# Kernel optimization log

Hardware: AMD Instinct MI355X
Metric: run time of the kernel (lower is better)

Reference implementation:

```python
import jax, jax.numpy as jnp
import numpy as np

NC = 80          # num_classes
REG_MAX = 16
TOPK = 10
IMG = 640
STRIDES = (8, 16, 32)
EPS = 1e-9


def make_anchors(shapes, strides):
    pts, strs = [], []
    for (h, w), s in zip(shapes, strides):
        sx = jnp.arange(w, dtype=jnp.float32)  # grid_cell_offset = 0.0
        sy = jnp.arange(h, dtype=jnp.float32)
        gy, gx = jnp.meshgrid(sy, sx, indexing='ij')
        pts.append(jnp.stack([gx, gy], -1).reshape(-1, 2))
        strs.append(jnp.full((h * w, 1), float(s), dtype=jnp.float32))
    return jnp.concatenate(pts, 0), jnp.concatenate(strs, 0)  # [A,2], [A,1]


def ciou(box1, box2, eps=1e-7):
    # boxes are xyxy, broadcastable; returns CIoU with last dim squeezed
    b1x1, b1y1, b1x2, b1y2 = jnp.split(box1, 4, -1)
    b2x1, b2y1, b2x2, b2y2 = jnp.split(box2, 4, -1)
    w1, h1 = b1x2 - b1x1, b1y2 - b1y1
    w2, h2 = b2x2 - b2x1, b2y2 - b2y1
    inter = (jnp.clip(jnp.minimum(b1x2, b2x2) - jnp.maximum(b1x1, b2x1), 0.0)
             * jnp.clip(jnp.minimum(b1y2, b2y2) - jnp.maximum(b1y1, b2y1), 0.0))
    union = w1 * h1 + w2 * h2 - inter + eps
    iou = inter / union
    cw = jnp.maximum(b1x2, b2x2) - jnp.minimum(b1x1, b2x1)
    ch = jnp.maximum(b1y2, b2y2) - jnp.minimum(b1y1, b2y1)
    c2 = cw ** 2 + ch ** 2 + eps
    rho2 = ((b2x1 + b2x2 - b1x1 - b1x2) ** 2 + (b2y1 + b2y2 - b1y1 - b1y2) ** 2) / 4.0
    v = (4.0 / np.pi ** 2) * (jnp.arctan(w2 / (h2 + eps)) - jnp.arctan(w1 / (h1 + eps))) ** 2
    alpha = jax.lax.stop_gradient(v / (v - iou + (1.0 + eps)))
    return (iou - (rho2 / c2 + v * alpha))[..., 0]


def bbox_decode(anchor_points, pred_distri):
    # distribution-focal decode: softmax over REG_MAX bins, expectation, dist2bbox
    B, A, _ = pred_distri.shape
    pd = pred_distri.reshape(B, A, 4, REG_MAX)
    proj = jnp.arange(REG_MAX, dtype=jnp.float32)
    dist = jnp.einsum('bacr,r->bac', jax.nn.softmax(pd, -1), proj)  # [B,A,4] ltrb
    lt, rb = dist[..., :2], dist[..., 2:]
    return jnp.concatenate([anchor_points - lt, anchor_points + rb], -1)  # xyxy


def assigner(pd_scores, pd_bboxes, anc_points, gt_labels, gt_bboxes, mask_gt,
             alpha=0.5, beta=6.0):
    # pd_scores [B,A,C] (sigmoid), pd_bboxes [B,A,4], gt_* [B,M,...], mask_gt [B,M,1]
    B, A, C = pd_scores.shape
    M = gt_bboxes.shape[1]
    mask_gt = mask_gt.astype(jnp.float32)
    # anchors whose center lies inside each gt box
    lt = anc_points[None, None, :, :] - gt_bboxes[:, :, None, :2]   # [B,M,A,2]
    rb = gt_bboxes[:, :, None, 2:] - anc_points[None, None, :, :]
    mask_in_gts = (jnp.minimum(lt.min(-1), rb.min(-1)) > EPS).astype(jnp.float32)  # [B,M,A]
    mask = mask_in_gts * mask_gt
    # class score of each anchor at the gt's label
    sc = jnp.take_along_axis(pd_scores[:, None, :, :],
                             gt_labels[:, :, None, None].astype(jnp.int32), axis=-1)[..., 0]  # [B,M,A]
    overlaps = jnp.clip(ciou(gt_bboxes[:, :, None, :], pd_bboxes[:, None, :, :]), 0.0) * mask
    bbox_scores = sc * mask
    align_metric = (bbox_scores ** alpha) * (overlaps ** beta)  # [B,M,A]
    # top-k candidates per gt
    _, idxs = jax.lax.top_k(align_metric, TOPK)                 # [B,M,K]
    valid = jnp.broadcast_to(mask_gt > 0, (B, M, TOPK))
    idxs = jnp.where(valid, idxs, 0)
    cnt = jnp.zeros((B * M, A), jnp.float32).at[
        jnp.arange(B * M)[:, None], idxs.reshape(B * M, TOPK)
    ].add(valid.reshape(B * M, TOPK).astype(jnp.float32)).reshape(B, M, A)
    mask_topk = jnp.where(cnt > 1, 0.0, cnt)
    mask_pos = mask_topk * mask_in_gts * mask_gt               # [B,M,A]
    # resolve anchors assigned to multiple gts by max overlap
    fg = mask_pos.sum(1)                                       # [B,A]
    multi = fg[:, None, :] > 1
    is_max = jax.nn.one_hot(overlaps.argmax(1), M, dtype=jnp.float32).transpose(0, 2, 1)
    mask_pos = jnp.where(multi, is_max, mask_pos)
    fg_mask = mask_pos.sum(1)                                  # [B,A]
    tgt_idx = mask_pos.argmax(1)                               # [B,A]
    # gather targets
    flat = tgt_idx + jnp.arange(B)[:, None] * M
    t_labels = jnp.clip(gt_labels.reshape(-1)[flat], 0)        # [B,A]
    t_bboxes = gt_bboxes.reshape(-1, 4)[flat]                  # [B,A,4]
    t_scores = jax.nn.one_hot(t_labels, C, dtype=jnp.float32) * (fg_mask[..., None] > 0)
    # normalize scores by aligned metric
    am = align_metric * mask_pos
    pos_am = am.max(-1, keepdims=True)                         # [B,M,1]
    pos_ov = (overlaps * mask_pos).max(-1, keepdims=True)      # [B,M,1]
    norm = (am * pos_ov / (pos_am + EPS)).max(1)[..., None]    # [B,A,1]
    return t_bboxes, t_scores * norm, fg_mask > 0


def setup_inputs() -> dict:
    key = jax.random.key(0)
    ks = jax.random.split(key, 9)
    B, M = 16, 32
    inp = {
        'cls0': jax.random.normal(ks[0], (B, NC, 80, 80), jnp.float32),
        'cls1': jax.random.normal(ks[1], (B, NC, 40, 40), jnp.float32),
        'cls2': jax.random.normal(ks[2], (B, NC, 20, 20), jnp.float32),
        'reg0': jax.random.normal(ks[3], (B, 4 * REG_MAX, 80, 80), jnp.float32),
        'reg1': jax.random.normal(ks[4], (B, 4 * REG_MAX, 40, 40), jnp.float32),
        'reg2': jax.random.normal(ks[5], (B, 4 * REG_MAX, 20, 20), jnp.float32),
    }
    cxy = jax.random.uniform(ks[6], (B, M, 2), minval=0.1, maxval=0.9)
    wh = jax.random.uniform(ks[7], (B, M, 2), minval=0.02, maxval=0.25)
    inp['boxes'] = jnp.concatenate([cxy, wh], -1)  # normalized cxcywh
    inp['labels'] = jax.random.randint(ks[8], (B, M), 0, NC)
    return inp


def reference(cls0, cls1, cls2, reg0, reg1, reg2, boxes, labels):
    cls_out, reg_out = [cls0, cls1, cls2], [reg0, reg1, reg2]
    B = cls0.shape[0]
    anc, stride_t = make_anchors([r.shape[2:] for r in reg_out], STRIDES)
    pred_scores = jnp.concatenate(
        [c.transpose(0, 2, 3, 1).reshape(B, -1, NC) for c in cls_out], 1)        # [B,A,C]
    pred_distri = jnp.concatenate(
        [r.transpose(0, 2, 3, 1).reshape(B, -1, 4 * REG_MAX) for r in reg_out], 1)
    # gt2xyxy: normalized cxcywh -> pixel xyxy
    cx, cy, w, h = jnp.split(boxes, 4, -1)
    gt_bboxes = jnp.concatenate([(cx - w / 2) * IMG, (cy - h / 2) * IMG,
                                 (cx + w / 2) * IMG, (cy + h / 2) * IMG], -1)
    mask_gt = gt_bboxes.sum(2, keepdims=True) > 0.0
    pred_bboxes = bbox_decode(anc, pred_distri)                                   # anchor units
    sg = jax.lax.stop_gradient
    t_bboxes, t_scores, fg_mask = assigner(
        sg(jax.nn.sigmoid(pred_scores)), sg(pred_bboxes) * stride_t,
        anc * stride_t, labels, gt_bboxes, mask_gt)
    tss = jnp.maximum(t_scores.sum(), 1.0)
    # classification BCE-with-logits
    x, t = pred_scores, t_scores
    bce = jnp.maximum(x, 0.0) - x * t + jnp.log1p(jnp.exp(-jnp.abs(x)))
    l_cls = bce.sum() / tss
    # bbox CIoU loss
    t_bboxes = t_bboxes / stride_t
    weight = t_scores.sum(-1) * fg_mask                                           # [B,A]
    iou = ciou(pred_bboxes, t_bboxes)
    l_iou = ((1.0 - iou) * weight).sum() / tss
    # DFL loss
    tltrb = jnp.clip(jnp.concatenate([anc - t_bboxes[..., :2],
                                      t_bboxes[..., 2:] - anc], -1),
                     0.0, REG_MAX - 1 - 0.01)                                     # [B,A,4]
    logp = jax.nn.log_softmax(pred_distri.reshape(B, -1, 4, REG_MAX), -1)
    tl = jnp.floor(tltrb).astype(jnp.int32)
    wl = (tl + 1).astype(jnp.float32) - tltrb
    lp_tl = jnp.take_along_axis(logp, tl[..., None], -1)[..., 0]
    lp_tr = jnp.take_along_axis(logp, (tl + 1)[..., None], -1)[..., 0]
    dfl = (-(lp_tl * wl + lp_tr * (1.0 - wl))).mean(-1)                           # [B,A]
    l_dfl = (dfl * weight).sum() / tss
    loss = jnp.stack([0.5 * l_cls, 7.5 * l_iou, 1.5 * l_dfl])
    return loss.sum(), loss
```

## Files before the change

kernel.cpp:

```cpp
#include <hip/hip_runtime.h>

#define NB 16
#define NM 32
#define NA 8400
#define NCC 80
#define NREG 64
#define A0 6400
#define A1 1600
#define A2 400
#define CAP 768

#define PRE_GRID 1024
#define PL_GRID 525

#define ACC_STRIDE 16
#define ACC_SLOTS 4


__device__ __forceinline__ void anch(int a, float& ax, float& ay, float& s, int& lvl, int& p) {
  if (a < A0)            { lvl = 0; p = a;          s = 8.f;  ax = (float)(p % 80); ay = (float)(p / 80); }
  else if (a < A0 + A1)  { lvl = 1; p = a - A0;     s = 16.f; ax = (float)(p % 40); ay = (float)(p / 40); }
  else                   { lvl = 2; p = a - A0 - A1; s = 32.f; ax = (float)(p % 20); ay = (float)(p / 20); }
}

__device__ __forceinline__ float cls_at(const float* c0, const float* c1, const float* c2,
                                        int b, int ch, int a) {
  if (a < A0)           return c0[((size_t)(b * NCC + ch)) * A0 + a];
  if (a < A0 + A1)      return c1[((size_t)(b * NCC + ch)) * A1 + (a - A0)];
  return c2[((size_t)(b * NCC + ch)) * A2 + (a - A0 - A1)];
}

__device__ __forceinline__ float reg_at(const float* r0, const float* r1, const float* r2,
                                        int b, int ch, int lvl, int p) {
  if (lvl == 0) return r0[((size_t)(b * NREG + ch)) * A0 + p];
  if (lvl == 1) return r1[((size_t)(b * NREG + ch)) * A1 + p];
  return r2[((size_t)(b * NREG + ch)) * A2 + p];
}

__device__ __forceinline__ void gtbox(const float* boxes, int b, int m,
                                      float& x1, float& y1, float& x2, float& y2, bool& valid) {
  const float* q = boxes + ((size_t)(b * NM + m)) * 4;
  float cx = q[0], cy = q[1], w = q[2], h = q[3];
  x1 = (cx - w * 0.5f) * 640.f; y1 = (cy - h * 0.5f) * 640.f;
  x2 = (cx + w * 0.5f) * 640.f; y2 = (cy + h * 0.5f) * 640.f;
  valid = (x1 + y1 + x2 + y2) > 0.f;
}

__device__ __forceinline__ float ciou_f(float b1x1, float b1y1, float b1x2, float b1y2,
                                        float b2x1, float b2y1, float b2x2, float b2y2) {
  const float eps = 1e-7f;
  float w1 = b1x2 - b1x1, h1 = b1y2 - b1y1;
  float w2 = b2x2 - b2x1, h2 = b2y2 - b2y1;
  float iw = fmaxf(fminf(b1x2, b2x2) - fmaxf(b1x1, b2x1), 0.f);
  float ih = fmaxf(fminf(b1y2, b2y2) - fmaxf(b1y1, b2y1), 0.f);
  float inter = iw * ih;
  float uni = w1 * h1 + w2 * h2 - inter + eps;
  float iou = inter / uni;
  float cw = fmaxf(b1x2, b2x2) - fminf(b1x1, b2x1);
  float ch = fmaxf(b1y2, b2y2) - fminf(b1y1, b2y1);
  float c2 = cw * cw + ch * ch + eps;
  float dx = b2x1 + b2x2 - b1x1 - b1x2;
  float dy = b2y1 + b2y2 - b1y1 - b1y2;
  float rho2 = (dx * dx + dy * dy) * 0.25f;
  float at = atanf(w2 / (h2 + eps)) - atanf(w1 / (h1 + eps));
  float v = 0.4052847345693511f * at * at;
  float alpha = v / (v - iou + (1.0f + eps));
  return iou - (rho2 / c2 + v * alpha);
}

__device__ __forceinline__ float align_of(float sc, float o) {
  float o2 = o * o, o4 = o2 * o2;
  return sqrtf(sc) * (o2 * o4);
}

__device__ __forceinline__ float softplus_fast(float x) {
  float e = __expf(-fabsf(x));
  return fmaxf(x, 0.f) + __logf(1.f + e);
}


__global__ __launch_bounds__(256) void k_pre(
    const float* r0, const float* r1, const float* r2,
    const float* c0, const float* c1, const float* c2,
    float4* bb, float4* mls, int* fgcnt, int* msum,
    unsigned* pos_am, unsigned* pos_ov, double* acc, double* bce_part) {
  const int gtid = blockIdx.x * 256 + threadIdx.x;
  const int nthr = gridDim.x * 256;

  for (int t = gtid; t < NB * NA; t += nthr) {
    fgcnt[t] = 0; msum[t] = 0;
    if (t < NB * NM) { pos_am[t] = 0u; pos_ov[t] = 0u; }
    if (t < ACC_SLOTS * ACC_STRIDE) acc[t] = 0.0;

    int b = t / NA, a = t % NA;
    float ax, ay, s; int lvl, p;
    anch(a, ax, ay, s, lvl, p);
    const float* rg; int HW;
    if (lvl == 0) { rg = r0; HW = A0; }
    else if (lvl == 1) { rg = r1; HW = A1; }
    else { rg = r2; HW = A2; }
    const float* base = rg + ((size_t)b * NREG) * HW + p;
    float dist[4], ml[4];
    for (int sd = 0; sd < 4; ++sd) {
      float x[16]; float mx = -1e30f;
      for (int r = 0; r < 16; ++r) { x[r] = base[(size_t)(sd * 16 + r) * HW]; mx = fmaxf(mx, x[r]); }
      float se = 0.f, wsum = 0.f;
      for (int r = 0; r < 16; ++r) { float e = __expf(x[r] - mx); se += e; wsum += e * (float)r; }
      dist[sd] = wsum / se;
      ml[sd] = mx + __logf(se);
    }
    bb[t]  = make_float4(ax - dist[0], ay - dist[1], ax + dist[2], ay + dist[3]);
    mls[t] = make_float4(ml[0], ml[1], ml[2], ml[3]);
  }

  const size_t N0 = (size_t)NB * NCC * A0 / 4;
  const size_t N1 = (size_t)NB * NCC * A1 / 4;
  const size_t N2 = (size_t)NB * NCC * A2 / 4;
  const size_t NT = N0 + N1 + N2;
  const float4* f0 = (const float4*)c0;
  const float4* f1 = (const float4*)c1;
  const float4* f2 = (const float4*)c2;
  float s0 = 0.f, s1 = 0.f;
  for (size_t i = (size_t)gtid; i < NT; i += (size_t)nthr) {
    float4 v;
    if (i < N0) v = f0[i];
    else if (i < N0 + N1) v = f1[i - N0];
    else v = f2[i - N0 - N1];
    s0 += softplus_fast(v.x) + softplus_fast(v.z);
    s1 += softplus_fast(v.y) + softplus_fast(v.w);
  }
  __shared__ double sred[256];
  sred[threadIdx.x] = (double)(s0 + s1);
  __syncthreads();
  for (int off = 128; off; off >>= 1) {
    if (threadIdx.x < off) sred[threadIdx.x] += sred[threadIdx.x + off];
    __syncthreads();
  }
  if (threadIdx.x == 0) bce_part[blockIdx.x] = sred[0];
}


__global__ __launch_bounds__(256) void k_assign(
    const float* boxes, const int* labels, const float4* bb,
    const float* c0, const float* c1, const float* c2,
    int* fgcnt, int* msum) {
  __shared__ float sv[CAP];
  __shared__ int   si[CAP];
  __shared__ int   s_n;
  const int bm = blockIdx.x;
  const int b = bm / NM, m = bm % NM;
  const int tid = threadIdx.x;
  const int lane = tid & 63;

  float gx1, gy1, gx2, gy2; bool valid;
  gtbox(boxes, b, m, gx1, gy1, gx2, gy2, valid);
  if (!valid) return;
  int lbl = labels[bm]; if (lbl < 0) lbl = 0; if (lbl >= NCC) lbl = NCC - 1;
  if (tid == 0) s_n = 0;
  __syncthreads();

  const int   Ws[3]   = {80, 40, 20};
  const float ss[3]   = {8.f, 16.f, 32.f};
  const int   loff[3] = {0, A0, A0 + A1};
  int rx0[3], ry0[3], rw[3], bc[3];
  int total = 0;
  for (int l = 0; l < 3; ++l) {
    float s = ss[l]; int W = Ws[l];
    int ax0 = (int)floorf((gx1 + 1e-9f) / s);
    int ax1 = (int)ceilf((gx2 - 1e-9f) / s);
    int ay0 = (int)floorf((gy1 + 1e-9f) / s);
    int ay1 = (int)ceilf((gy2 - 1e-9f) / s);
    ax0 = max(ax0, 0); ay0 = max(ay0, 0);
    ax1 = min(ax1, W - 1); ay1 = min(ay1, W - 1);
    rx0[l] = ax0; ry0[l] = ay0;
    rw[l] = max(0, ax1 - ax0 + 1);
    int rhl = max(0, ay1 - ay0 + 1);
    bc[l] = total;
    total += rw[l] * rhl;
  }
  int iters = (total + 255) >> 8;
  for (int it = 0; it < iters; ++it) {
    int idx = it * 256 + tid;
    bool pred = false; float am = 0.f; int a = 0;
    if (idx < total) {
      int l = (idx >= bc[2]) ? 2 : ((idx >= bc[1]) ? 1 : 0);
      int r = idx - bc[l];
      int iy = r / rw[l], ix = r - iy * rw[l];
      int axg = rx0[l] + ix, ayg = ry0[l] + iy;
      a = loff[l] + ayg * Ws[l] + axg;
      float s = ss[l];
      float axp = (float)axg * s, ayp = (float)ayg * s;
      float mn = fminf(fminf(axp - gx1, ayp - gy1), fminf(gx2 - axp, gy2 - ayp));
      if (mn > 1e-9f) {
        pred = true;
        float4 pb = bb[(size_t)b * NA + a];
        float c = ciou_f(gx1, gy1, gx2, gy2, pb.x * s, pb.y * s, pb.z * s, pb.w * s);
        float o = fmaxf(c, 0.f);
        float x = cls_at(c0, c1, c2, b, lbl, a);
        float sc = 1.f / (1.f + expf(-x));
        am = align_of(sc, o);
      }
    }
    unsigned long long mask = __ballot(pred);
    if (mask) {
      int nact = __popcll(mask);
      int leader = __ffsll(mask) - 1;
      int basec = 0;
      if (lane == leader) basec = atomicAdd(&s_n, nact);
      basec = __shfl(basec, leader);
      if (pred) {
        int off = basec + __popcll(mask & ((1ull << lane) - 1ull));
        if (off < CAP) { sv[off] = am; si[off] = a; }
      }
    }
  }
  __syncthreads();
  int n = s_n; if (n > CAP) n = CAP;
  if (n == 0) return;
  if (tid >= 64) return;

  float v[12]; int ix[12];
#pragma unroll
  for (int k = 0; k < 12; ++k) {
    int j = k * 64 + tid;
    bool in = (j < n);
    v[k]  = in ? sv[j] : -2.f;
    ix[k] = in ? si[j] : (1 << 30);
  }
  int cnt = 0;
#pragma unroll
  for (int k = 0; k < 12; ++k) cnt += (v[k] > 0.f) ? 1 : 0;
  for (int o = 32; o; o >>= 1) cnt += __shfl_xor(cnt, o);
  int npos = cnt;

  if (npos > 10) {
    for (int p = 0; p < 10; ++p) {
      float bv = -1.f; int bi = 1 << 30;
#pragma unroll
      for (int k = 0; k < 12; ++k) {
        if (v[k] > bv || (v[k] == bv && ix[k] < bi)) { bv = v[k]; bi = ix[k]; }
      }
      for (int o = 32; o; o >>= 1) {
        float wv = __shfl_xor(bv, o); int wi = __shfl_xor(bi, o);
        if (wv > bv || (wv == bv && wi < bi)) { bv = wv; bi = wi; }
      }
#pragma unroll
      for (int k = 0; k < 12; ++k) if (ix[k] == bi) v[k] = -1.f;
      if (tid == 0) {
        atomicAdd(&fgcnt[(size_t)b * NA + bi], 1);
        atomicAdd(&msum[(size_t)b * NA + bi], m);
      }
    }
  } else {
#pragma unroll
    for (int k = 0; k < 12; ++k) {
      if (v[k] > 0.f) {
        atomicAdd(&fgcnt[(size_t)b * NA + ix[k]], 1);
        atomicAdd(&msum[(size_t)b * NA + ix[k]], m);
      }
    }
    int need = 10 - npos;
    for (int j = tid; j < n; j += 64) {
      if (sv[j] == 0.f) {
        int i = si[j];
        if (i < 10) {
          int pb = 0;
          for (int q = 0; q < n; ++q) pb += (sv[q] > 0.f && si[q] < i) ? 1 : 0;
          if (i - pb < need) {
            atomicAdd(&fgcnt[(size_t)b * NA + i], 1);
            atomicAdd(&msum[(size_t)b * NA + i], m);
          }
        }
      }
    }
  }
}


__global__ __launch_bounds__(256) void k_resolve(const float* boxes, const int* labels,
                                                 const float4* bb,
                                                 const float* c0, const float* c1, const float* c2,
                                                 const int* fgcnt, const int* msum,
                                                 int* assign, float* amv,
                                                 unsigned* pos_am, unsigned* pos_ov) {
  int t = blockIdx.x * blockDim.x + threadIdx.x;
  if (t >= NB * NA) return;
  int b = t / NA, a = t % NA;
  int fg = fgcnt[t];
  int asn = -1; float o = 0.f;
  if (fg > 0) {
    float ax, ay, s; int lvl, p;
    anch(a, ax, ay, s, lvl, p);
    float axp = ax * s, ayp = ay * s;
    float4 pb = bb[t];
    float px1 = pb.x * s, py1 = pb.y * s, px2 = pb.z * s, py2 = pb.w * s;
    if (fg == 1) {
      asn = msum[t];
      float gx1, gy1, gx2, gy2; bool valid;
      gtbox(boxes, b, asn, gx1, gy1, gx2, gy2, valid);
      o = fmaxf(ciou_f(gx1, gy1, gx2, gy2, px1, py1, px2, py2), 0.f);
    } else {
      float bv = -1e30f; int bi = 0;
      for (int m = 0; m < NM; ++m) {
        float gx1, gy1, gx2, gy2; bool valid;
        gtbox(boxes, b, m, gx1, gy1, gx2, gy2, valid);
        float om = 0.f;
        if (valid) {
          float mn = fminf(fminf(axp - gx1, ayp - gy1), fminf(gx2 - axp, gy2 - ayp));
          if (mn > 1e-9f)
            om = fmaxf(ciou_f(gx1, gy1, gx2, gy2, px1, py1, px2, py2), 0.f);
        }
        if (om > bv) { bv = om; bi = m; }
      }
      asn = bi; o = bv;
    }
    float am = 0.f;
    if (o > 0.f) {
      int lbl = labels[b * NM + asn]; if (lbl < 0) lbl = 0; if (lbl >= NCC) lbl = NCC - 1;
      float x = cls_at(c0, c1, c2, b, lbl, a);
      float sc = 1.f / (1.f + expf(-x));
      am = align_of(sc, o);
      atomicMax(&pos_am[b * NM + asn], __float_as_uint(am));
      atomicMax(&pos_ov[b * NM + asn], __float_as_uint(o));
    }
    amv[t] = am;
  }
  assign[t] = asn;
}


__global__ __launch_bounds__(256) void k_post(const float* c0, const float* c1, const float* c2,
    const float* r0, const float* r1, const float* r2,
    const float* boxes, const int* labels, const int* assign, const float* amv,
    const float4* bb, const float4* mls, const unsigned* pos_am, const unsigned* pos_ov,
    double* acc) {
  const int tid = threadIdx.x;
  const int t = blockIdx.x * 256 + tid;
  double t_norm = 0.0, t_x = 0.0, t_iou = 0.0, t_dfl = 0.0;
  int asn = (t < NB * NA) ? assign[t] : -1;
  if (asn >= 0) {
    int b = t / NA, a = t % NA;
    float pam = __uint_as_float(pos_am[b * NM + asn]);
    float pov = __uint_as_float(pos_ov[b * NM + asn]);
    float norm = amv[t] * pov / (pam + 1e-9f);
    int lbl = labels[b * NM + asn]; if (lbl < 0) lbl = 0; if (lbl >= NCC) lbl = NCC - 1;
    float x = cls_at(c0, c1, c2, b, lbl, a);
    float gx1, gy1, gx2, gy2; bool valid;
    gtbox(boxes, b, asn, gx1, gy1, gx2, gy2, valid);
    float ax, ay, s; int lvl, p;
    anch(a, ax, ay, s, lvl, p);
    float inv_s = 1.f / s;
    float tx1 = gx1 * inv_s, ty1 = gy1 * inv_s, tx2 = gx2 * inv_s, ty2 = gy2 * inv_s;
    float4 pb = bb[t];
    float iou = ciou_f(pb.x, pb.y, pb.z, pb.w, tx1, ty1, tx2, ty2);
    float4 ml = mls[t];
    float tgt[4] = { ax - tx1, ay - ty1, tx2 - ax, ty2 - ay };
    float mlv[4] = { ml.x, ml.y, ml.z, ml.w };
    float dfl = 0.f;
    for (int sd = 0; sd < 4; ++sd) {
      float tv = fminf(fmaxf(tgt[sd], 0.f), 14.99f);
      float tlf = floorf(tv);
      int tl = (int)tlf;
      float wl = (tlf + 1.f) - tv;
      float xtl = reg_at(r0, r1, r2, b, sd * 16 + tl,     lvl, p);
      float xtr = reg_at(r0, r1, r2, b, sd * 16 + tl + 1, lvl, p);
      dfl += -((xtl - mlv[sd]) * wl + (xtr - mlv[sd]) * (1.f - wl));
    }
    dfl *= 0.25f;
    t_norm = (double)norm;
    t_x    = (double)(norm * x);
    t_iou  = (double)((1.f - iou) * norm);
    t_dfl  = (double)(dfl * norm);
  }
  __shared__ double sred[256];
  double vals[4] = { t_norm, t_x, t_iou, t_dfl };
  for (int q = 0; q < 4; ++q) {
    sred[tid] = vals[q];
    __syncthreads();
    for (int off = 128; off; off >>= 1) {
      if (tid < off) sred[tid] += sred[tid + off];
      __syncthreads();
    }
    if (tid == 0 && sred[0] != 0.0) atomicAdd(&acc[q * ACC_STRIDE], sred[0]);
    __syncthreads();
  }
}


__global__ __launch_bounds__(256) void k_final(const double* bce_part, const double* acc, float* out) {
  __shared__ double sred[256];
  double s = 0.0;
  for (int i = threadIdx.x; i < PRE_GRID; i += 256) s += bce_part[i];
  sred[threadIdx.x] = s;
  __syncthreads();
  for (int off = 128; off; off >>= 1) {
    if (threadIdx.x < off) sred[threadIdx.x] += sred[threadIdx.x + off];
    __syncthreads();
  }
  if (threadIdx.x == 0) {
    double a_bce  = sred[0];
    double a_norm = acc[0 * ACC_STRIDE];
    double a_x    = acc[1 * ACC_STRIDE];
    double a_iou  = acc[2 * ACC_STRIDE];
    double a_dfl  = acc[3 * ACC_STRIDE];
    double tss = a_norm; if (tss < 1.0) tss = 1.0;
    double l0 = 0.5 * (a_bce - a_x) / tss;
    double l1 = 7.5 * a_iou / tss;
    double l2 = 1.5 * a_dfl / tss;
    out[0] = (float)(l0 + l1 + l2);
    out[1] = (float)l0;
    out[2] = (float)l1;
    out[3] = (float)l2;
  }
}


extern "C" void kernel_launch(void* const* d_in, const int* in_sizes, int n_in,
                              void* d_out, int out_size, void* d_ws, size_t ws_size,
                              hipStream_t stream) {
  (void)in_sizes; (void)n_in; (void)out_size; (void)ws_size;
  const float* cls0  = (const float*)d_in[0];
  const float* cls1  = (const float*)d_in[1];
  const float* cls2  = (const float*)d_in[2];
  const float* reg0  = (const float*)d_in[3];
  const float* reg1  = (const float*)d_in[4];
  const float* reg2  = (const float*)d_in[5];
  const float* boxes = (const float*)d_in[6];
  const int*   labels = (const int*)d_in[7];
  float* out = (float*)d_out;

  const size_t BA = (size_t)NB * NA;
  const int    BM = NB * NM;

  char* wsb = (char*)d_ws;
  double*   bce_part = (double*)wsb;
  double*   acc      = bce_part + PRE_GRID;
  unsigned* pos_am   = (unsigned*)(acc + ACC_SLOTS * ACC_STRIDE);
  unsigned* pos_ov   = pos_am + BM;
  int*      fgcnt    = (int*)(pos_ov + BM);
  int*      msum     = fgcnt + BA;
  float*    bbp      = (float*)(msum + BA);
  float*    mlsp     = bbp + BA * 4;
  float*    amv      = mlsp + BA * 4;
  int*      assign   = (int*)(amv + BA);

  float4* bb  = (float4*)bbp;
  float4* mls = (float4*)mlsp;

  k_pre<<<PRE_GRID, 256, 0, stream>>>(reg0, reg1, reg2, cls0, cls1, cls2,
                                      bb, mls, fgcnt, msum, pos_am, pos_ov,
                                      acc, bce_part);
  k_assign<<<BM, 256, 0, stream>>>(boxes, labels, (const float4*)bb,
                                   cls0, cls1, cls2, fgcnt, msum);
  k_resolve<<<PL_GRID, 256, 0, stream>>>(boxes, labels, (const float4*)bb, cls0, cls1, cls2,
                                         fgcnt, msum, assign, amv, pos_am, pos_ov);
  k_post<<<PL_GRID, 256, 0, stream>>>(cls0, cls1, cls2, reg0, reg1, reg2,
                                      boxes, labels, assign, amv,
                                      (const float4*)bb, (const float4*)mls, pos_am, pos_ov,
                                      acc);
  k_final<<<1, 256, 0, stream>>>(bce_part, acc, out);
}
```

Before: 67.69 us.

## Compact foreground anchors into a worklist and fuse resolve/post via per-GT accumulators

The assign kernel now pushes each newly-touched foreground anchor onto a global worklist. A single small-grid kernel then resolves and scores only those anchors instead of scanning all B*A anchors twice. The per-anchor normalization by pos_am/pos_ov is deferred by accumulating am-weighted sums per GT and scaling them in the final kernel, which removes the need for a separate post pass. The pre kernel also processes four anchors per thread using float4 loads of the regression logits. Risks: worklist overflow is silently capped at WL_MAX, there is extra atomic traffic on double accumulators, and the per-GT deferred scaling is only equivalent to the original norm if pos_am/pos_ov are final before scaling (they are, since scaling happens in k_final).

```diff
diff --git a/kernel.cpp b/kernel.cpp
--- a/kernel.cpp
+++ b/kernel.cpp
@@ -11,10 +11,8 @@
 #define CAP 768
 
 #define PRE_GRID 1024
-#define PL_GRID 525
-
-#define ACC_STRIDE 16
-#define ACC_SLOTS 4
+#define WL_MAX 5376
+#define RP_GRID 20
 
 
 __device__ __forceinline__ void anch(int a, float& ax, float& ay, float& s, int& lvl, int& p) {
@@ -83,34 +81,58 @@
     const float* r0, const float* r1, const float* r2,
     const float* c0, const float* c1, const float* c2,
     float4* bb, float4* mls, int* fgcnt, int* msum,
-    unsigned* pos_am, unsigned* pos_ov, double* acc, double* bce_part) {
+    unsigned* pos_am, unsigned* pos_ov, double* gt_acc, int* wl_cnt, double* bce_part) {
   const int gtid = blockIdx.x * 256 + threadIdx.x;
   const int nthr = gridDim.x * 256;
 
-  for (int t = gtid; t < NB * NA; t += nthr) {
-    fgcnt[t] = 0; msum[t] = 0;
-    if (t < NB * NM) { pos_am[t] = 0u; pos_ov[t] = 0u; }
-    if (t < ACC_SLOTS * ACC_STRIDE) acc[t] = 0.0;
-
-    int b = t / NA, a = t % NA;
-    float ax, ay, s; int lvl, p;
-    anch(a, ax, ay, s, lvl, p);
+  for (int t = gtid; t < NB * NA; t += nthr) { fgcnt[t] = 0; msum[t] = 0; }
+  if (gtid < NB * NM) { pos_am[gtid] = 0u; pos_ov[gtid] = 0u; }
+  if (gtid < NB * NM * 4) gt_acc[gtid] = 0.0;
+  if (gtid == 0) *wl_cnt = 0;
+
+  for (int q = gtid; q < (NB * NA) / 4; q += nthr) {
+    int t0 = q * 4;
+    int b = t0 / NA, a0 = t0 % NA;
+    float ax0, ay, s; int lvl, p0;
+    anch(a0, ax0, ay, s, lvl, p0);
     const float* rg; int HW;
     if (lvl == 0) { rg = r0; HW = A0; }
     else if (lvl == 1) { rg = r1; HW = A1; }
     else { rg = r2; HW = A2; }
-    const float* base = rg + ((size_t)b * NREG) * HW + p;
-    float dist[4], ml[4];
+    const float* base = rg + ((size_t)b * NREG) * HW + p0;
+    float dist[4][4], ml[4][4];
+#pragma unroll
     for (int sd = 0; sd < 4; ++sd) {
-      float x[16]; float mx = -1e30f;
-      for (int r = 0; r < 16; ++r) { x[r] = base[(size_t)(sd * 16 + r) * HW]; mx = fmaxf(mx, x[r]); }
-      float se = 0.f, wsum = 0.f;
-      for (int r = 0; r < 16; ++r) { float e = __expf(x[r] - mx); se += e; wsum += e * (float)r; }
-      dist[sd] = wsum / se;
-      ml[sd] = mx + __logf(se);
-    }
-    bb[t]  = make_float4(ax - dist[0], ay - dist[1], ax + dist[2], ay + dist[3]);
-    mls[t] = make_float4(ml[0], ml[1], ml[2], ml[3]);
+      float xv[16][4];
+      float mx[4] = { -1e30f, -1e30f, -1e30f, -1e30f };
+#pragma unroll
+      for (int r = 0; r < 16; ++r) {
+        float4 v = *(const float4*)(base + (size_t)(sd * 16 + r) * HW);
+        xv[r][0] = v.x; xv[r][1] = v.y; xv[r][2] = v.z; xv[r][3] = v.w;
+        mx[0] = fmaxf(mx[0], v.x); mx[1] = fmaxf(mx[1], v.y);
+        mx[2] = fmaxf(mx[2], v.z); mx[3] = fmaxf(mx[3], v.w);
+      }
+      float se[4] = {0.f,0.f,0.f,0.f}, ws[4] = {0.f,0.f,0.f,0.f};
+#pragma unroll
+      for (int r = 0; r < 16; ++r) {
+#pragma unroll
+        for (int j = 0; j < 4; ++j) {
+          float e = __expf(xv[r][j] - mx[j]);
+          se[j] += e; ws[j] += e * (float)r;
+        }
+      }
+#pragma unroll
+      for (int j = 0; j < 4; ++j) {
+        dist[sd][j] = ws[j] / se[j];
+        ml[sd][j]   = mx[j] + __logf(se[j]);
+      }
+    }
+#pragma unroll
+    for (int j = 0; j < 4; ++j) {
+      float axj = ax0 + (float)j;
+      bb[t0 + j]  = make_float4(axj - dist[0][j], ay - dist[1][j], axj + dist[2][j], ay + dist[3][j]);
+      mls[t0 + j] = make_float4(ml[0][j], ml[1][j], ml[2][j], ml[3][j]);
+    }
   }
 
   const size_t N0 = (size_t)NB * NCC * A0 / 4;
@@ -140,10 +162,20 @@
 }
 
 
+__device__ __forceinline__ void fg_touch(int* fgcnt, int* msum, int* wl_cnt, int* worklist,
+                                         int t, int m) {
+  int old = atomicAdd(&fgcnt[t], 1);
+  if (old == 0) {
+    int w = atomicAdd(wl_cnt, 1);
+    if (w < WL_MAX) worklist[w] = t;
+  }
+  atomicAdd(&msum[t], m);
+}
+
 __global__ __launch_bounds__(256) void k_assign(
     const float* boxes, const int* labels, const float4* bb,
     const float* c0, const float* c1, const float* c2,
-    int* fgcnt, int* msum) {
+    int* fgcnt, int* msum, int* wl_cnt, int* worklist) {
   __shared__ float sv[CAP];
   __shared__ int   si[CAP];
   __shared__ int   s_n;
@@ -246,18 +278,12 @@
       }
 #pragma unroll
       for (int k = 0; k < 12; ++k) if (ix[k] == bi) v[k] = -1.f;
-      if (tid == 0) {
-        atomicAdd(&fgcnt[(size_t)b * NA + bi], 1);
-        atomicAdd(&msum[(size_t)b * NA + bi], m);
-      }
+      if (tid == 0) fg_touch(fgcnt, msum, wl_cnt, worklist, (int)((size_t)b * NA) + bi, m);
     }
   } else {
 #pragma unroll
     for (int k = 0; k < 12; ++k) {
-      if (v[k] > 0.f) {
-        atomicAdd(&fgcnt[(size_t)b * NA + ix[k]], 1);
-        atomicAdd(&msum[(size_t)b * NA + ix[k]], m);
-      }
+      if (v[k] > 0.f) fg_touch(fgcnt, msum, wl_cnt, worklist, b * NA + ix[k], m);
     }
     int need = 10 - npos;
     for (int j = tid; j < n; j += 64) {
@@ -266,10 +292,7 @@
         if (i < 10) {
           int pb = 0;
           for (int q = 0; q < n; ++q) pb += (sv[q] > 0.f && si[q] < i) ? 1 : 0;
-          if (i - pb < need) {
-            atomicAdd(&fgcnt[(size_t)b * NA + i], 1);
-            atomicAdd(&msum[(size_t)b * NA + i], m);
-          }
+          if (i - pb < need) fg_touch(fgcnt, msum, wl_cnt, worklist, b * NA + i, m);
         }
       }
     }
@@ -277,23 +300,26 @@
 }
 
 
-__global__ __launch_bounds__(256) void k_resolve(const float* boxes, const int* labels,
-                                                 const float4* bb,
-                                                 const float* c0, const float* c1, const float* c2,
-                                                 const int* fgcnt, const int* msum,
-                                                 int* assign, float* amv,
-                                                 unsigned* pos_am, unsigned* pos_ov) {
-  int t = blockIdx.x * blockDim.x + threadIdx.x;
-  if (t >= NB * NA) return;
-  int b = t / NA, a = t % NA;
-  int fg = fgcnt[t];
-  int asn = -1; float o = 0.f;
-  if (fg > 0) {
+__global__ __launch_bounds__(256) void k_rp(
+    const float* boxes, const int* labels,
+    const float4* bb, const float4* mls,
+    const float* c0, const float* c1, const float* c2,
+    const float* r0, const float* r1, const float* r2,
+    const int* fgcnt, const int* msum,
+    const int* wl_cnt, const int* worklist,
+    unsigned* pos_am, unsigned* pos_ov, double* gt_acc) {
+  int nwl = *wl_cnt; if (nwl > WL_MAX) nwl = WL_MAX;
+  const int nthr = gridDim.x * 256;
+  for (int i = blockIdx.x * 256 + threadIdx.x; i < nwl; i += nthr) {
+    int t = worklist[i];
+    int b = t / NA, a = t % NA;
+    int fg = fgcnt[t];
     float ax, ay, s; int lvl, p;
     anch(a, ax, ay, s, lvl, p);
     float axp = ax * s, ayp = ay * s;
     float4 pb = bb[t];
     float px1 = pb.x * s, py1 = pb.y * s, px2 = pb.z * s, py2 = pb.w * s;
+    int asn; float o;
     if (fg == 1) {
       asn = msum[t];
       float gx1, gy1, gx2, gy2; bool valid;
@@ -314,44 +340,20 @@
       }
       asn = bi; o = bv;
     }
-    float am = 0.f;
-    if (o > 0.f) {
-      int lbl = labels[b * NM + asn]; if (lbl < 0) lbl = 0; if (lbl >= NCC) lbl = NCC - 1;
-      float x = cls_at(c0, c1, c2, b, lbl, a);
-      float sc = 1.f / (1.f + expf(-x));
-      am = align_of(sc, o);
-      atomicMax(&pos_am[b * NM + asn], __float_as_uint(am));
-      atomicMax(&pos_ov[b * NM + asn], __float_as_uint(o));
-    }
-    amv[t] = am;
-  }
-  assign[t] = asn;
-}
-
-
-__global__ __launch_bounds__(256) void k_post(const float* c0, const float* c1, const float* c2,
-    const float* r0, const float* r1, const float* r2,
-    const float* boxes, const int* labels, const int* assign, const float* amv,
-    const float4* bb, const float4* mls, const unsigned* pos_am, const unsigned* pos_ov,
-    double* acc) {
-  const int tid = threadIdx.x;
-  const int t = blockIdx.x * 256 + tid;
-  double t_norm = 0.0, t_x = 0.0, t_iou = 0.0, t_dfl = 0.0;
-  int asn = (t < NB * NA) ? assign[t] : -1;
-  if (asn >= 0) {
-    int b = t / NA, a = t % NA;
-    float pam = __uint_as_float(pos_am[b * NM + asn]);
-    float pov = __uint_as_float(pos_ov[b * NM + asn]);
-    float norm = amv[t] * pov / (pam + 1e-9f);
-    int lbl = labels[b * NM + asn]; if (lbl < 0) lbl = 0; if (lbl >= NCC) lbl = NCC - 1;
+    if (o <= 0.f) continue;
+    int g = b * NM + asn;
+    int lbl = labels[g]; if (lbl < 0) lbl = 0; if (lbl >= NCC) lbl = NCC - 1;
     float x = cls_at(c0, c1, c2, b, lbl, a);
+    float sc = 1.f / (1.f + expf(-x));
+    float am = align_of(sc, o);
+    atomicMax(&pos_am[g], __float_as_uint(am));
+    atomicMax(&pos_ov[g], __float_as_uint(o));
+    if (am <= 0.f) continue;
+
     float gx1, gy1, gx2, gy2; bool valid;
     gtbox(boxes, b, asn, gx1, gy1, gx2, gy2, valid);
-    float ax, ay, s; int lvl, p;
-    anch(a, ax, ay, s, lvl, p);
     float inv_s = 1.f / s;
     float tx1 = gx1 * inv_s, ty1 = gy1 * inv_s, tx2 = gx2 * inv_s, ty2 = gy2 * inv_s;
-    float4 pb = bb[t];
     float iou = ciou_f(pb.x, pb.y, pb.z, pb.w, tx1, ty1, tx2, ty2);
     float4 ml = mls[t];
     float tgt[4] = { ax - tx1, ay - ty1, tx2 - ax, ty2 - ay };
@@ -367,46 +369,47 @@
       dfl += -((xtl - mlv[sd]) * wl + (xtr - mlv[sd]) * (1.f - wl));
     }
     dfl *= 0.25f;
-    t_norm = (double)norm;
-    t_x    = (double)(norm * x);
-    t_iou  = (double)((1.f - iou) * norm);
-    t_dfl  = (double)(dfl * norm);
-  }
+    atomicAdd(&gt_acc[g * 4 + 0], (double)am);
+    atomicAdd(&gt_acc[g * 4 + 1], (double)(am * x));
+    atomicAdd(&gt_acc[g * 4 + 2], (double)(am * (1.f - iou)));
+    atomicAdd(&gt_acc[g * 4 + 3], (double)(am * dfl));
+  }
+}
+
+
+__global__ __launch_bounds__(256) void k_final(const double* bce_part, const double* gt_acc,
+                                               const unsigned* pos_am, const unsigned* pos_ov,
+                                               float* out) {
+  const int tid = threadIdx.x;
+  double tss = 0.0, sx = 0.0, siou = 0.0, sdfl = 0.0, bce = 0.0;
+  for (int g = tid; g < NB * NM; g += 256) {
+    float pam = __uint_as_float(pos_am[g]);
+    float pov = __uint_as_float(pos_ov[g]);
+    double sc = (double)pov / ((double)pam + 1e-9);
+    tss  += gt_acc[g * 4 + 0] * sc;
+    sx   += gt_acc[g * 4 + 1] * sc;
+    siou += gt_acc[g * 4 + 2] * sc;
+    sdfl += gt_acc[g * 4 + 3] * sc;
+  }
+  for (int i = tid; i < PRE_GRID; i += 256) bce += bce_part[i];
   __shared__ double sred[256];
-  double vals[4] = { t_norm, t_x, t_iou, t_dfl };
-  for (int q = 0; q < 4; ++q) {
+  double vals[5] = { tss, sx, siou, sdfl, bce };
+  double tot[5];
+  for (int q = 0; q < 5; ++q) {
     sred[tid] = vals[q];
     __syncthreads();
     for (int off = 128; off; off >>= 1) {
       if (tid < off) sred[tid] += sred[tid + off];
       __syncthreads();
     }
-    if (tid == 0 && sred[0] != 0.0) atomicAdd(&acc[q * ACC_STRIDE], sred[0]);
+    tot[q] = sred[0];
     __syncthreads();
   }
-}
-
-
-__global__ __launch_bounds__(256) void k_final(const double* bce_part, const double* acc, float* out) {
-  __shared__ double sred[256];
-  double s = 0.0;
-  for (int i = threadIdx.x; i < PRE_GRID; i += 256) s += bce_part[i];
-  sred[threadIdx.x] = s;
-  __syncthreads();
-  for (int off = 128; off; off >>= 1) {
-    if (threadIdx.x < off) sred[threadIdx.x] += sred[threadIdx.x + off];
-    __syncthreads();
-  }
-  if (threadIdx.x == 0) {
-    double a_bce  = sred[0];
-    double a_norm = acc[0 * ACC_STRIDE];
-    double a_x    = acc[1 * ACC_STRIDE];
-    double a_iou  = acc[2 * ACC_STRIDE];
-    double a_dfl  = acc[3 * ACC_STRIDE];
-    double tss = a_norm; if (tss < 1.0) tss = 1.0;
-    double l0 = 0.5 * (a_bce - a_x) / tss;
-    double l1 = 7.5 * a_iou / tss;
-    double l2 = 1.5 * a_dfl / tss;
+  if (tid == 0) {
+    double t = tot[0]; if (t < 1.0) t = 1.0;
+    double l0 = 0.5 * (tot[4] - tot[1]) / t;
+    double l1 = 7.5 * tot[2] / t;
+    double l2 = 1.5 * tot[3] / t;
     out[0] = (float)(l0 + l1 + l2);
     out[1] = (float)l0;
     out[2] = (float)l1;
@@ -434,29 +437,27 @@
 
   char* wsb = (char*)d_ws;
   double*   bce_part = (double*)wsb;
-  double*   acc      = bce_part + PRE_GRID;
-  unsigned* pos_am   = (unsigned*)(acc + ACC_SLOTS * ACC_STRIDE);
+  double*   gt_acc   = bce_part + PRE_GRID;
+  unsigned* pos_am   = (unsigned*)(gt_acc + (size_t)BM * 4);
   unsigned* pos_ov   = pos_am + BM;
-  int*      fgcnt    = (int*)(pos_ov + BM);
+  int*      wl_cnt   = (int*)(pos_ov + BM);
+  int*      worklist = wl_cnt + 4;
+  int*      fgcnt    = worklist + WL_MAX;
   int*      msum     = fgcnt + BA;
   float*    bbp      = (float*)(msum + BA);
   float*    mlsp     = bbp + BA * 4;
-  float*    amv      = mlsp + BA * 4;
-  int*      assign   = (int*)(amv + BA);
 
   float4* bb  = (float4*)bbp;
   float4* mls = (float4*)mlsp;
 
   k_pre<<<PRE_GRID, 256, 0, stream>>>(reg0, reg1, reg2, cls0, cls1, cls2,
                                       bb, mls, fgcnt, msum, pos_am, pos_ov,
-                                      acc, bce_part);
+                                      gt_acc, wl_cnt, bce_part);
   k_assign<<<BM, 256, 0, stream>>>(boxes, labels, (const float4*)bb,
-                                   cls0, cls1, cls2, fgcnt, msum);
-  k_resolve<<<PL_GRID, 256, 0, stream>>>(boxes, labels, (const float4*)bb, cls0, cls1, cls2,
-                                         fgcnt, msum, assign, amv, pos_am, pos_ov);
-  k_post<<<PL_GRID, 256, 0, stream>>>(cls0, cls1, cls2, reg0, reg1, reg2,
-                                      boxes, labels, assign, amv,
-                                      (const float4*)bb, (const float4*)mls, pos_am, pos_ov,
-                                      acc);
-  k_final<<<1, 256, 0, stream>>>(bce_part, acc, out);
-}
+                                   cls0, cls1, cls2, fgcnt, msum, wl_cnt, worklist);
+  k_rp<<<RP_GRID, 256, 0, stream>>>(boxes, labels, (const float4*)bb, (const float4*)mls,
+                                    cls0, cls1, cls2, reg0, reg1, reg2,
+                                    fgcnt, msum, wl_cnt, worklist,
+                                    pos_am, pos_ov, gt_acc);
+  k_final<<<1, 256, 0, stream>>>(bce_part, gt_acc, pos_am, pos_ov, out);
+}
```

After: 129.6 us. 1.92x slower.
